# Optimization experiments

Measured on AMD Instinct MI355X. Metric: run time of the kernel, lower is better.

The kernel has to match this reference:

```python
import jax, jax.numpy as jnp
import numpy as np

D_MODEL = 512
NUM_HEADS = 8
D_K = D_MODEL // NUM_HEADS
SCALE = float(np.sqrt(D_K))


def setup_inputs() -> dict:
    key = jax.random.key(0)
    ks = jax.random.split(key, 11)
    B, S, D = 2, 4096, D_MODEL
    std = 1.0 / np.sqrt(D)
    return {
        "query": jax.random.normal(ks[0], (B, S, D), jnp.float32),
        "key": jax.random.normal(ks[1], (B, S, D), jnp.float32),
        "value": jax.random.normal(ks[2], (B, S, D), jnp.float32),
        "w_q": jax.random.normal(ks[3], (D, D), jnp.float32) * std,
        "b_q": jax.random.normal(ks[4], (D,), jnp.float32) * std,
        "w_k": jax.random.normal(ks[5], (D, D), jnp.float32) * std,
        "b_k": jax.random.normal(ks[6], (D,), jnp.float32) * std,
        "w_v": jax.random.normal(ks[7], (D, D), jnp.float32) * std,
        "b_v": jax.random.normal(ks[8], (D,), jnp.float32) * std,
        "w_o": jax.random.normal(ks[9], (D, D), jnp.float32) * std,
        "b_o": jax.random.normal(ks[10], (D,), jnp.float32) * std,
    }


def reference(query, key, value, w_q, b_q, w_k, b_k, w_v, b_v, w_o, b_o):
    B, S, D = query.shape
    H, Dk = NUM_HEADS, D_K
    # Linear projections (torch Linear: x @ W^T + b), split into heads -> [B,H,S,Dk]
    Q = (query @ w_q.T + b_q).reshape(B, S, H, Dk).transpose(0, 2, 1, 3)
    K = (key @ w_k.T + b_k).reshape(B, S, H, Dk).transpose(0, 2, 1, 3)
    V = (value @ w_v.T + b_v).reshape(B, S, H, Dk).transpose(0, 2, 1, 3)
    # [B,H,S,S] attention scores — intentionally materialized like the original
    scores = jnp.einsum("bhqd,bhkd->bhqk", Q, K) / SCALE
    attn = jax.nn.softmax(scores, axis=-1)  # dropout rate 0 in eval baseline
    attended = jnp.einsum("bhqk,bhkd->bhqd", attn, V)
    attended = attended.transpose(0, 2, 1, 3).reshape(B, S, D)
    return attended @ w_o.T + b_o
```

## Files before the change

### kernel.cpp

```cpp
#include <hip/hip_runtime.h>
#include <math.h>

#define D_MODEL 512
#define NHEADS 8
#define DK 64
#define BATCH 2
#define SEQ 4096
#define NIT 32
#define ATTN_SCALE 0.18033688011112043f
#define SPLIT_SCALE 2048.0f
#define INV_SPLIT  (1.0f/2048.0f)

typedef _Float16 half8 __attribute__((ext_vector_type(8)));
typedef __fp16 pkhalf2 __attribute__((ext_vector_type(2)));
typedef float f32x4 __attribute__((ext_vector_type(4)));

union Pk8 { _Float16 h[8]; uint4 u; };
union Pk4 { _Float16 h[4]; uint2 u; };
union Pkz { pkhalf2 h2[2]; uint2 u; };
union Un4 { uint2 u; _Float16 h[4]; };

#if __has_builtin(__builtin_amdgcn_exp2f)
#define EXP2F __builtin_amdgcn_exp2f
#else
#define EXP2F exp2f
#endif

#define MFMA16(a, b, c) __builtin_amdgcn_mfma_f32_16x16x32_f16((a), (b), (c), 0, 0, 0)

__device__ __forceinline__ void gload_lds16(const _Float16* g, _Float16* l) {
    __builtin_amdgcn_global_load_lds(
        (const __attribute__((address_space(1))) void*)g,
        (__attribute__((address_space(3))) void*)l, 16, 0, 0);
}

#define ABLK 4096
#define WBLK 256
__global__ __launch_bounds__(256)
void prep(const float* __restrict__ aq, const float* __restrict__ ak,
          const float* __restrict__ av,
          const float* __restrict__ wq, const float* __restrict__ wk,
          const float* __restrict__ wv, const float* __restrict__ wo,
          _Float16* __restrict__ dq, _Float16* __restrict__ dk,
          _Float16* __restrict__ dv,
          _Float16* __restrict__ hq, _Float16* __restrict__ hk,
          _Float16* __restrict__ hv, _Float16* __restrict__ ho) {
    int gid = blockIdx.x;
    const float* src;
    _Float16* hi;
    if (gid < 3 * ABLK) {
        const int w = gid / ABLK;
        gid -= w * ABLK;
        src = w == 0 ? aq : (w == 1 ? ak : av);
        hi  = w == 0 ? dq : (w == 1 ? dk : dv);
    } else {
        int g = gid - 3 * ABLK;
        const int w = g / WBLK;
        gid = g - w * WBLK;
        src = w == 0 ? wq : (w == 1 ? wk : (w == 2 ? wv : wo));
        hi  = w == 0 ? hq : (w == 1 ? hk : (w == 2 ? hv : ho));
    }
    const int i = (gid * 256 + threadIdx.x) * 4;
    float4 v = *(const float4*)(src + i);
    Pkz h;
    h.h2[0] = __builtin_amdgcn_cvt_pkrtz(v.x, v.y);
    h.h2[1] = __builtin_amdgcn_cvt_pkrtz(v.z, v.w);
    *(uint2*)(hi + i) = h.u;
}

__global__ __launch_bounds__(256)
void gemm_qkv(const _Float16* __restrict__ Aq, const _Float16* __restrict__ Ak,
              const _Float16* __restrict__ Av,
              const _Float16* __restrict__ Whq, const _Float16* __restrict__ Whk,
              const _Float16* __restrict__ Whv,
              const float* __restrict__ bq, const float* __restrict__ bk,
              const float* __restrict__ bv,
              _Float16* __restrict__ Qf, _Float16* __restrict__ Kf,
              _Float16* __restrict__ Vtf) {
    const int z = blockIdx.z;
    const _Float16* A    = z == 0 ? Aq  : (z == 1 ? Ak  : Av);
    const _Float16* Wh   = z == 0 ? Whq : (z == 1 ? Whk : Whv);
    const float*    bias = z == 0 ? bq  : (z == 1 ? bk  : bv);

    __shared__ __align__(16) _Float16 sA[2][128 * 64];
    __shared__ __align__(16) _Float16 sW[2][128 * 64];

    const int t    = threadIdx.x;
    const int lane = t & 63, wave = t >> 6;
    const int col  = lane & 15, quad = lane >> 4;
    const int wm   = (wave & 1) * 64, wn = (wave >> 1) * 64;
    const int m0   = blockIdx.y * 128, n0 = blockIdx.x * 128;

    const int subrow = lane >> 3;
    const int schunk = ((lane & 7) ^ subrow) * 8;

    #define STAGE_AW(K0, BUF)                                                        \
        do {                                                                          \
            _Pragma("unroll")                                                         \
            for (int j = 0; j < 4; ++j) {                                             \
                const int rw = wave * 32 + j * 8;                                     \
                gload_lds16(A  + (size_t)(m0 + rw + subrow) * 512 + (K0) + schunk,    \
                            &sA[BUF][rw * 64]);                                       \
                gload_lds16(Wh + (size_t)(n0 + rw + subrow) * 512 + (K0) + schunk,    \
                            &sW[BUF][rw * 64]);                                       \
            }                                                                         \
        } while (0)

    f32x4 acc[4][4] = {};

    STAGE_AW(0, 0);
    for (int ck = 0; ck < 8; ++ck) {
        const int cur = ck & 1;
        __syncthreads();
        if (ck + 1 < 8) STAGE_AW((ck + 1) * 64, cur ^ 1);

        #pragma unroll
        for (int kc = 0; kc < 2; ++kc) {
            const int pos = ((kc * 4 + quad) ^ (col & 7)) * 8;
            half8 af[4], wf[4];
            #pragma unroll
            for (int mt = 0; mt < 4; ++mt)
                af[mt] = *(const half8*)&sA[cur][(wm + mt * 16 + col) * 64 + pos];
            #pragma unroll
            for (int nt = 0; nt < 4; ++nt)
                wf[nt] = *(const half8*)&sW[cur][(wn + nt * 16 + col) * 64 + pos];
            #pragma unroll
            for (int mt = 0; mt < 4; ++mt)
                #pragma unroll
                for (int nt = 0; nt < 4; ++nt)
                    acc[mt][nt] = MFMA16(af[mt], wf[nt], acc[mt][nt]);
        }
    }

    float bv4[4];
    #pragma unroll
    for (int nt = 0; nt < 4; ++nt) bv4[nt] = bias[n0 + wn + nt * 16 + col];

    if (z < 2) {
        _Float16* Out = z == 0 ? Qf : Kf;
        const float alpha = z == 0 ? ATTN_SCALE : 1.0f;
        #pragma unroll
        for (int mt = 0; mt < 4; ++mt) {
            const int m = m0 + wm + mt * 16 + quad * 4;
            #pragma unroll
            for (int nt = 0; nt < 4; ++nt) {
                const int n = n0 + wn + nt * 16 + col;
                #pragma unroll
                for (int r = 0; r < 4; ++r)
                    Out[(size_t)(m + r) * 512 + n] = (_Float16)((acc[mt][nt][r] + bv4[nt]) * alpha);
            }
        }
    } else {
        #pragma unroll
        for (int mt = 0; mt < 4; ++mt) {
            const int m = m0 + wm + mt * 16 + quad * 4;
            const int b = m >> 12, s = m & (SEQ - 1);
            #pragma unroll
            for (int nt = 0; nt < 4; ++nt) {
                const int n = n0 + wn + nt * 16 + col;
                const int hh = n >> 6, d = n & (DK - 1);
                Pk4 p;
                #pragma unroll
                for (int r = 0; r < 4; ++r)
                    p.h[r] = (_Float16)(acc[mt][nt][r] + bv4[nt]);
                *(uint2*)&Vtf[((size_t)((b * NHEADS + hh) * DK + d)) * SEQ + s] = p.u;
            }
        }
    }
}

__global__ __launch_bounds__(256)
void attn_mfma(const _Float16* __restrict__ Qf, const _Float16* __restrict__ Kf,
               const _Float16* __restrict__ Vtf,
               _Float16* __restrict__ Op0, _Float16* __restrict__ Op1,
               float2* __restrict__ Ml) {
    __shared__ __align__(16) _Float16 sK[2][64 * 64];
    __shared__ __align__(16) _Float16 sV[64 * 64];
    __shared__ __align__(16) _Float16 sP[128 * 64];

    const int t    = threadIdx.x;
    const int lane = t & 63;
    const int wave = t >> 6;
    const int col  = lane & 15;
    const int quad = lane >> 4;

    const int strm = blockIdx.x;
    const int h  = strm & (NHEADS - 1);
    const int z  = strm >> 3;
    const int b  = z >> 1;
    const int sp = z & 1;
    const int q0 = blockIdx.y * 128;
    const int kBase = sp * (SEQ / 2);

    const size_t rowBase = (size_t)b * SEQ;
    const size_t vBase   = ((size_t)(b * NHEADS + h)) * DK * SEQ;

    const int subrow = lane >> 3;
    const int schunk = ((lane & 7) ^ subrow) * 8;
    const _Float16* kP[2];
    const _Float16* vP[2];
    #pragma unroll
    for (int j = 0; j < 2; ++j) {
        const int rw = wave * 16 + j * 8;
        kP[j] = Kf + (rowBase + kBase + rw + subrow) * 512 + h * 64 + schunk;
        vP[j] = Vtf + vBase + (size_t)(rw + subrow) * SEQ + kBase + schunk;
        gload_lds16(kP[j], &sK[0][rw * 64]);
        kP[j] += 64 * 512;
    }

    {
        uint4 qv[4];
        #pragma unroll
        for (int i2 = 0; i2 < 4; ++i2) {
            const int slot = t + i2 * 256;
            const int r = slot >> 3, sl = slot & 7;
            qv[i2] = *(const uint4*)(Qf + (rowBase + q0 + r) * 512 + h * 64 + sl * 8);
        }
        #pragma unroll
        for (int i2 = 0; i2 < 4; ++i2) {
            const int slot = t + i2 * 256;
            const int r = slot >> 3, sl = slot & 7;
            *(uint4*)&sP[r * 64 + (sl ^ (r & 7)) * 8] = qv[i2];
        }
    }
    __syncthreads();

    half8 qf[2][2];
    #pragma unroll
    for (int nt = 0; nt < 2; ++nt)
        #pragma unroll
        for (int kc = 0; kc < 2; ++kc)
            qf[nt][kc] = *(const half8*)&sP[(wave * 32 + nt * 16 + col) * 64 +
                                            ((kc * 4 + quad) ^ (col & 7)) * 8];

    _Float16* Ps = sP + wave * 32 * 64;
    const int pmsk = (col & 7) << 1;

    float m_r[2] = { -INFINITY, -INFINITY };
    float l_r[2] = { 0.0f, 0.0f };
    f32x4 of[4][2] = {};

    for (int itp = 0; itp < NIT; itp += 2) {
        #pragma unroll
        for (int cur = 0; cur < 2; ++cur) {
            const int it = itp + cur;
            __syncthreads();
            #pragma unroll
            for (int j = 0; j < 2; ++j) {
                const int rw = wave * 16 + j * 8;
                gload_lds16(vP[j], &sV[rw * 64]);
                vP[j] += 64;
            }
            if (it + 1 < NIT) {
                #pragma unroll
                for (int j = 0; j < 2; ++j) {
                    const int rw = wave * 16 + j * 8;
                    gload_lds16(kP[j], &sK[cur ^ 1][rw * 64]);
                    kP[j] += 64 * 512;
                }
            }

            f32x4 sf[4][2] = {};
            #pragma unroll
            for (int kc = 0; kc < 2; ++kc) {
                const int pos = ((kc * 4 + quad) ^ (col & 7)) * 8;
                #pragma unroll
                for (int kt = 0; kt < 4; ++kt) {
                    half8 kf = *(const half8*)&sK[cur][(kt * 16 + col) * 64 + pos];
                    #pragma unroll
                    for (int nt = 0; nt < 2; ++nt)
                        sf[kt][nt] = MFMA16(kf, qf[nt][kc], sf[kt][nt]);
                }
            }

            if (it == 0) {
                #pragma unroll
                for (int nt = 0; nt < 2; ++nt) {
                    float mx = sf[0][nt][0];
                    #pragma unroll
                    for (int kt = 0; kt < 4; ++kt)
                        #pragma unroll
                        for (int r = 0; r < 4; ++r)
                            mx = fmaxf(mx, sf[kt][nt][r]);
                    mx = fmaxf(mx, __shfl_xor(mx, 16));
                    mx = fmaxf(mx, __shfl_xor(mx, 32));
                    m_r[nt] = mx;
                }
            }

            float lrs[2];
            #pragma unroll
            for (int nt = 0; nt < 2; ++nt) {
                float ls = 0.0f;
                #pragma unroll
                for (int kt = 0; kt < 4; ++kt) {
                    const float p0 = EXP2F(sf[kt][nt][0] - m_r[nt]);
                    const float p1 = EXP2F(sf[kt][nt][1] - m_r[nt]);
                    const float p2 = EXP2F(sf[kt][nt][2] - m_r[nt]);
                    const float p3 = EXP2F(sf[kt][nt][3] - m_r[nt]);
                    ls += (p0 + p1) + (p2 + p3);
                    Pkz z2;
                    z2.h2[0] = __builtin_amdgcn_cvt_pkrtz(p0, p1);
                    z2.h2[1] = __builtin_amdgcn_cvt_pkrtz(p2, p3);
                    *(uint2*)&Ps[(nt * 16 + col) * 64 + ((kt * 4 + quad) ^ pmsk) * 4] = z2.u;
                }
                lrs[nt] = ls;
            }

            __syncthreads();

            #pragma unroll
            for (int kc = 0; kc < 2; ++kc) {
                half8 pf[2];
                #pragma unroll
                for (int nt = 0; nt < 2; ++nt)
                    pf[nt] = *(const half8*)&Ps[(nt * 16 + col) * 64 +
                                                ((kc * 8 + quad * 2) ^ pmsk) * 4];
                const int pos = ((kc * 4 + quad) ^ (col & 7)) * 8;
                #pragma unroll
                for (int dt = 0; dt < 4; ++dt) {
                    half8 vf = *(const half8*)&sV[(dt * 16 + col) * 64 + pos];
                    of[dt][0] = MFMA16(vf, pf[0], of[dt][0]);
                    of[dt][1] = MFMA16(vf, pf[1], of[dt][1]);
                }
            }

            l_r[0] += lrs[0];
            l_r[1] += lrs[1];

            if (__any(fmaxf(lrs[0], lrs[1]) > 1024.0f)) {
                #pragma unroll
                for (int nt = 0; nt < 2; ++nt) {
                    float mx = sf[0][nt][0];
                    #pragma unroll
                    for (int kt = 0; kt < 4; ++kt)
                        #pragma unroll
                        for (int r = 0; r < 4; ++r)
                            mx = fmaxf(mx, sf[kt][nt][r]);
                    mx = fmaxf(mx, __shfl_xor(mx, 16));
                    mx = fmaxf(mx, __shfl_xor(mx, 32));
                    if (mx > m_r[nt]) {
                        const float al = EXP2F(m_r[nt] - mx);
                        l_r[nt] *= al;
                        #pragma unroll
                        for (int dt = 0; dt < 4; ++dt)
                            #pragma unroll
                            for (int r = 0; r < 4; ++r)
                                of[dt][nt][r] *= al;
                        m_r[nt] = mx;
                    }
                }
            }
        }
    }

    _Float16* Opx = sp ? Op1 : Op0;
    #pragma unroll
    for (int nt = 0; nt < 2; ++nt) {
        float l = l_r[nt];
        l += __shfl_xor(l, 16);
        l += __shfl_xor(l, 32);
        const float inv = 1.0f / l;
        const int q = q0 + wave * 32 + nt * 16 + col;
        const size_t R = (size_t)b * SEQ + q;
        #pragma unroll
        for (int dt = 0; dt < 4; ++dt) {
            Pkz z2;
            z2.h2[0] = __builtin_amdgcn_cvt_pkrtz(of[dt][nt][0] * inv, of[dt][nt][1] * inv);
            z2.h2[1] = __builtin_amdgcn_cvt_pkrtz(of[dt][nt][2] * inv, of[dt][nt][3] * inv);
            *(uint2*)(Opx + R * 512 + h * 64 + dt * 16 + quad * 4) = z2.u;
        }
        if (quad == 0)
            Ml[(size_t)(sp * BATCH * SEQ) * NHEADS + R * NHEADS + h] = make_float2(m_r[nt], l);
    }
}

__global__ __launch_bounds__(256)
void attn_merge(const _Float16* __restrict__ Op0, const _Float16* __restrict__ Op1,
                const float2* __restrict__ Ml, _Float16* __restrict__ Oh) {
    const int i4 = (blockIdx.x * 256 + threadIdx.x) * 4;
    const int R = i4 >> 9;
    const int c = i4 & 511;
    const int h = c >> 6;

    const float2 ml1 = Ml[(size_t)R * NHEADS + h];
    const float2 ml2 = Ml[(size_t)(BATCH * SEQ) * NHEADS + (size_t)R * NHEADS + h];
    const float m = fmaxf(ml1.x, ml2.x);
    float w1 = EXP2F(ml1.x - m) * ml1.y;
    float w2 = EXP2F(ml2.x - m) * ml2.y;
    const float inv = 1.0f / (w1 + w2);
    w1 *= inv; w2 *= inv;

    Un4 a, bb;
    a.u  = *(const uint2*)(Op0 + (size_t)R * 512 + c);
    bb.u = *(const uint2*)(Op1 + (size_t)R * 512 + c);

    Pkz hh;
    hh.h2[0] = __builtin_amdgcn_cvt_pkrtz(w1 * (float)a.h[0] + w2 * (float)bb.h[0],
                                          w1 * (float)a.h[1] + w2 * (float)bb.h[1]);
    hh.h2[1] = __builtin_amdgcn_cvt_pkrtz(w1 * (float)a.h[2] + w2 * (float)bb.h[2],
                                          w1 * (float)a.h[3] + w2 * (float)bb.h[3]);
    *(uint2*)(Oh + (size_t)R * 512 + c) = hh.u;
}

__global__ __launch_bounds__(256)
void gemm_out(const _Float16* __restrict__ Ah, const _Float16* __restrict__ Wh,
              const float* __restrict__ bias, float* __restrict__ C) {
    __shared__ __align__(16) _Float16 sAh[2][128 * 64];
    __shared__ __align__(16) _Float16 sWh[2][64 * 64];

    const int t    = threadIdx.x;
    const int lane = t & 63, wave = t >> 6;
    const int col  = lane & 15, quad = lane >> 4;
    const int wm   = (wave & 1) * 64, wn = (wave >> 1) * 32;
    const int m0   = blockIdx.y * 128, n0 = blockIdx.x * 64;

    const int subrow = lane >> 3;
    const int schunk = ((lane & 7) ^ subrow) * 8;

    #define STAGE_OUT(K0, BUF)                                                       \
        do {                                                                          \
            _Pragma("unroll")                                                         \
            for (int j = 0; j < 4; ++j) {                                             \
                const int rw = wave * 32 + j * 8;                                     \
                gload_lds16(Ah + (size_t)(m0 + rw + subrow) * 512 + (K0) + schunk,    \
                            &sAh[BUF][rw * 64]);                                      \
            }                                                                         \
            _Pragma("unroll")                                                         \
            for (int j = 0; j < 2; ++j) {                                             \
                const int rw = wave * 16 + j * 8;                                     \
                gload_lds16(Wh + (size_t)(n0 + rw + subrow) * 512 + (K0) + schunk,    \
                            &sWh[BUF][rw * 64]);                                      \
            }                                                                         \
        } while (0)

    f32x4 acc[4][2] = {};

    STAGE_OUT(0, 0);
    for (int ck = 0; ck < 8; ++ck) {
        const int cur = ck & 1;
        __syncthreads();
        if (ck + 1 < 8) STAGE_OUT((ck + 1) * 64, cur ^ 1);

        #pragma unroll
        for (int kc = 0; kc < 2; ++kc) {
            const int pos = ((kc * 4 + quad) ^ (col & 7)) * 8;
            half8 ahf[4], whf[2];
            #pragma unroll
            for (int mt = 0; mt < 4; ++mt)
                ahf[mt] = *(const half8*)&sAh[cur][(wm + mt * 16 + col) * 64 + pos];
            #pragma unroll
            for (int nt = 0; nt < 2; ++nt)
                whf[nt] = *(const half8*)&sWh[cur][(wn + nt * 16 + col) * 64 + pos];
            #pragma unroll
            for (int mt = 0; mt < 4; ++mt)
                #pragma unroll
                for (int nt = 0; nt < 2; ++nt)
                    acc[mt][nt] = MFMA16(ahf[mt], whf[nt], acc[mt][nt]);
        }
    }

    float bv2[2];
    #pragma unroll
    for (int nt = 0; nt < 2; ++nt) bv2[nt] = bias[n0 + wn + nt * 16 + col];

    #pragma unroll
    for (int mt = 0; mt < 4; ++mt) {
        const int m = m0 + wm + mt * 16 + quad * 4;
        #pragma unroll
        for (int nt = 0; nt < 2; ++nt) {
            const int n = n0 + wn + nt * 16 + col;
            #pragma unroll
            for (int r = 0; r < 4; ++r)
                C[(size_t)(m + r) * 512 + n] = acc[mt][nt][r] + bv2[nt];
        }
    }
}

extern "C" void kernel_launch(void* const* d_in, const int* in_sizes, int n_in,
                              void* d_out, int out_size, void* d_ws, size_t ws_size,
                              hipStream_t stream) {
    const float* query = (const float*)d_in[0];
    const float* key   = (const float*)d_in[1];
    const float* value = (const float*)d_in[2];
    const float* w_q   = (const float*)d_in[3];
    const float* b_q   = (const float*)d_in[4];
    const float* w_k   = (const float*)d_in[5];
    const float* b_k   = (const float*)d_in[6];
    const float* w_v   = (const float*)d_in[7];
    const float* b_v   = (const float*)d_in[8];
    const float* w_o   = (const float*)d_in[9];
    const float* b_o   = (const float*)d_in[10];
    float* out = (float*)d_out;

    const int WN = D_MODEL * D_MODEL;
    const size_t plane = (size_t)BATCH * SEQ * D_MODEL;

    _Float16* base = (_Float16*)d_ws;
    _Float16* Aq16 = base;
    _Float16* Ak16 = Aq16 + plane;
    _Float16* Av16 = Ak16 + plane;
    _Float16* whq  = Av16 + plane;
    _Float16* whk  = whq + WN;
    _Float16* whv  = whk + WN;
    _Float16* who  = whv + WN;
    _Float16* Qf   = who + WN;
    _Float16* Kf   = Qf + plane;
    _Float16* Vtf  = Kf + plane;
    _Float16* Op1  = Vtf + plane;
    float2*   Ml   = (float2*)(Op1 + plane);
    _Float16* Oh   = Aq16;
    _Float16* Op0  = Av16;

    dim3 blk(256);

    hipLaunchKernelGGL(prep, dim3(3 * ABLK + 4 * WBLK), blk, 0, stream,
                       query, key, value, w_q, w_k, w_v, w_o,
                       Aq16, Ak16, Av16, whq, whk, whv, who);

    hipLaunchKernelGGL(gemm_qkv, dim3(D_MODEL / 128, BATCH * SEQ / 128, 3), blk, 0, stream,
                       Aq16, Ak16, Av16,
                       whq, whk, whv,
                       b_q, b_k, b_v, Qf, Kf, Vtf);

    hipLaunchKernelGGL(attn_mfma, dim3(NHEADS * BATCH * 2, SEQ / 128), blk, 0, stream,
                       Qf, Kf, Vtf, Op0, Op1, Ml);

    hipLaunchKernelGGL(attn_merge, dim3(BATCH * SEQ * D_MODEL / 4 / 256), blk, 0, stream,
                       Op0, Op1, Ml, Oh);

    hipLaunchKernelGGL(gemm_out, dim3(D_MODEL / 64, BATCH * SEQ / 128), blk, 0, stream,
                       Oh, who, b_o, out);
}
```

Baseline: 257.0 us.

## Double-buffer V tiles, per-wave P buffers, fold max into MFMA accumulator init

V tiles are now double-buffered and prefetched one iteration ahead together with K. The per-wave P staging drops to a 32x32 buffer written and read in two halves, which removes the block-wide barrier between softmax and PV. Q fragments load directly from global instead of through LDS, and the running max is subtracted by seeding the QK accumulator with -m. s_setprio hints wrap the MFMA sections. These aim to cut barriers and LDS traffic and to overlap loads, at the cost of more LDS for V and reliance on wave-local ordering of the P writes and reads.

```diff
diff --git a/kernel.cpp b/kernel.cpp
--- a/kernel.cpp
+++ b/kernel.cpp
@@ -8,8 +8,6 @@
 #define SEQ 4096
 #define NIT 32
 #define ATTN_SCALE 0.18033688011112043f
-#define SPLIT_SCALE 2048.0f
-#define INV_SPLIT  (1.0f/2048.0f)
 
 typedef _Float16 half8 __attribute__((ext_vector_type(8)));
 typedef __fp16 pkhalf2 __attribute__((ext_vector_type(2)));
@@ -32,6 +30,10 @@
     __builtin_amdgcn_global_load_lds(
         (const __attribute__((address_space(1))) void*)g,
         (__attribute__((address_space(3))) void*)l, 16, 0, 0);
+}
+
+__device__ __forceinline__ f32x4 splat4(float v) {
+    return (f32x4){v, v, v, v};
 }
 
 #define ABLK 4096
@@ -175,8 +177,8 @@
                _Float16* __restrict__ Op0, _Float16* __restrict__ Op1,
                float2* __restrict__ Ml) {
     __shared__ __align__(16) _Float16 sK[2][64 * 64];
-    __shared__ __align__(16) _Float16 sV[64 * 64];
-    __shared__ __align__(16) _Float16 sP[128 * 64];
+    __shared__ __align__(16) _Float16 sV[2][64 * 64];
+    __shared__ __align__(16) _Float16 sP[4][32 * 32];
 
     const int t    = threadIdx.x;
     const int lane = t & 63;
@@ -205,38 +207,25 @@
         kP[j] = Kf + (rowBase + kBase + rw + subrow) * 512 + h * 64 + schunk;
         vP[j] = Vtf + vBase + (size_t)(rw + subrow) * SEQ + kBase + schunk;
         gload_lds16(kP[j], &sK[0][rw * 64]);
+        gload_lds16(vP[j], &sV[0][rw * 64]);
         kP[j] += 64 * 512;
-    }
-
-    {
-        uint4 qv[4];
-        #pragma unroll
-        for (int i2 = 0; i2 < 4; ++i2) {
-            const int slot = t + i2 * 256;
-            const int r = slot >> 3, sl = slot & 7;
-            qv[i2] = *(const uint4*)(Qf + (rowBase + q0 + r) * 512 + h * 64 + sl * 8);
-        }
-        #pragma unroll
-        for (int i2 = 0; i2 < 4; ++i2) {
-            const int slot = t + i2 * 256;
-            const int r = slot >> 3, sl = slot & 7;
-            *(uint4*)&sP[r * 64 + (sl ^ (r & 7)) * 8] = qv[i2];
-        }
-    }
-    __syncthreads();
+        vP[j] += 64;
+    }
 
     half8 qf[2][2];
     #pragma unroll
     for (int nt = 0; nt < 2; ++nt)
         #pragma unroll
         for (int kc = 0; kc < 2; ++kc)
-            qf[nt][kc] = *(const half8*)&sP[(wave * 32 + nt * 16 + col) * 64 +
-                                            ((kc * 4 + quad) ^ (col & 7)) * 8];
-
-    _Float16* Ps = sP + wave * 32 * 64;
-    const int pmsk = (col & 7) << 1;
-
-    float m_r[2] = { -INFINITY, -INFINITY };
+            qf[nt][kc] = *(const half8*)(Qf +
+                (rowBase + q0 + wave * 32 + nt * 16 + col) * 512 +
+                h * 64 + (kc * 4 + quad) * 8);
+
+    _Float16* Ps = sP[wave];
+    const int c3   = (col & 3) << 1;
+    const int cmsk = col & 7;
+
+    float m_r[2] = { 0.0f, 0.0f };
     float l_r[2] = { 0.0f, 0.0f };
     f32x4 of[4][2] = {};
 
@@ -245,33 +234,35 @@
         for (int cur = 0; cur < 2; ++cur) {
             const int it = itp + cur;
             __syncthreads();
-            #pragma unroll
-            for (int j = 0; j < 2; ++j) {
-                const int rw = wave * 16 + j * 8;
-                gload_lds16(vP[j], &sV[rw * 64]);
-                vP[j] += 64;
-            }
             if (it + 1 < NIT) {
                 #pragma unroll
                 for (int j = 0; j < 2; ++j) {
                     const int rw = wave * 16 + j * 8;
                     gload_lds16(kP[j], &sK[cur ^ 1][rw * 64]);
+                    gload_lds16(vP[j], &sV[cur ^ 1][rw * 64]);
                     kP[j] += 64 * 512;
+                    vP[j] += 64;
                 }
             }
 
-            f32x4 sf[4][2] = {};
+            f32x4 sf[4][2];
+            #pragma unroll
+            for (int kt = 0; kt < 4; ++kt) {
+                sf[kt][0] = splat4(-m_r[0]);
+                sf[kt][1] = splat4(-m_r[1]);
+            }
+            __builtin_amdgcn_s_setprio(1);
             #pragma unroll
             for (int kc = 0; kc < 2; ++kc) {
-                const int pos = ((kc * 4 + quad) ^ (col & 7)) * 8;
+                const int pos = ((kc * 4 + quad) ^ cmsk) * 8;
                 #pragma unroll
                 for (int kt = 0; kt < 4; ++kt) {
                     half8 kf = *(const half8*)&sK[cur][(kt * 16 + col) * 64 + pos];
-                    #pragma unroll
-                    for (int nt = 0; nt < 2; ++nt)
-                        sf[kt][nt] = MFMA16(kf, qf[nt][kc], sf[kt][nt]);
+                    sf[kt][0] = MFMA16(kf, qf[0][kc], sf[kt][0]);
+                    sf[kt][1] = MFMA16(kf, qf[1][kc], sf[kt][1]);
                 }
             }
+            __builtin_amdgcn_s_setprio(0);
 
             if (it == 0) {
                 #pragma unroll
@@ -285,44 +276,48 @@
                     mx = fmaxf(mx, __shfl_xor(mx, 16));
                     mx = fmaxf(mx, __shfl_xor(mx, 32));
                     m_r[nt] = mx;
+                    #pragma unroll
+                    for (int kt = 0; kt < 4; ++kt)
+                        #pragma unroll
+                        for (int r = 0; r < 4; ++r)
+                            sf[kt][nt][r] -= mx;
                 }
             }
 
-            float lrs[2];
-            #pragma unroll
-            for (int nt = 0; nt < 2; ++nt) {
-                float ls = 0.0f;
-                #pragma unroll
-                for (int kt = 0; kt < 4; ++kt) {
-                    const float p0 = EXP2F(sf[kt][nt][0] - m_r[nt]);
-                    const float p1 = EXP2F(sf[kt][nt][1] - m_r[nt]);
-                    const float p2 = EXP2F(sf[kt][nt][2] - m_r[nt]);
-                    const float p3 = EXP2F(sf[kt][nt][3] - m_r[nt]);
-                    ls += (p0 + p1) + (p2 + p3);
-                    Pkz z2;
-                    z2.h2[0] = __builtin_amdgcn_cvt_pkrtz(p0, p1);
-                    z2.h2[1] = __builtin_amdgcn_cvt_pkrtz(p2, p3);
-                    *(uint2*)&Ps[(nt * 16 + col) * 64 + ((kt * 4 + quad) ^ pmsk) * 4] = z2.u;
+            float lrs[2] = { 0.0f, 0.0f };
+            #pragma unroll
+            for (int kh = 0; kh < 2; ++kh) {
+                #pragma unroll
+                for (int kt2 = 0; kt2 < 2; ++kt2) {
+                    const int kt = kh * 2 + kt2;
+                    #pragma unroll
+                    for (int nt = 0; nt < 2; ++nt) {
+                        const float p0 = EXP2F(sf[kt][nt][0]);
+                        const float p1 = EXP2F(sf[kt][nt][1]);
+                        const float p2 = EXP2F(sf[kt][nt][2]);
+                        const float p3 = EXP2F(sf[kt][nt][3]);
+                        lrs[nt] += (p0 + p1) + (p2 + p3);
+                        Pkz z2;
+                        z2.h2[0] = __builtin_amdgcn_cvt_pkrtz(p0, p1);
+                        z2.h2[1] = __builtin_amdgcn_cvt_pkrtz(p2, p3);
+                        *(uint2*)&Ps[(nt * 16 + col) * 32 +
+                                     (((kt2 * 4 + quad) ^ c3) << 2)] = z2.u;
+                    }
                 }
-                lrs[nt] = ls;
-            }
-
-            __syncthreads();
-
-            #pragma unroll
-            for (int kc = 0; kc < 2; ++kc) {
                 half8 pf[2];
                 #pragma unroll
                 for (int nt = 0; nt < 2; ++nt)
-                    pf[nt] = *(const half8*)&Ps[(nt * 16 + col) * 64 +
-                                                ((kc * 8 + quad * 2) ^ pmsk) * 4];
-                const int pos = ((kc * 4 + quad) ^ (col & 7)) * 8;
+                    pf[nt] = *(const half8*)&Ps[(nt * 16 + col) * 32 +
+                                                (((quad * 2) ^ c3) << 2)];
+                const int pos = ((kh * 4 + quad) ^ cmsk) * 8;
+                __builtin_amdgcn_s_setprio(1);
                 #pragma unroll
                 for (int dt = 0; dt < 4; ++dt) {
-                    half8 vf = *(const half8*)&sV[(dt * 16 + col) * 64 + pos];
+                    half8 vf = *(const half8*)&sV[cur][(dt * 16 + col) * 64 + pos];
                     of[dt][0] = MFMA16(vf, pf[0], of[dt][0]);
                     of[dt][1] = MFMA16(vf, pf[1], of[dt][1]);
                 }
+                __builtin_amdgcn_s_setprio(0);
             }
 
             l_r[0] += lrs[0];
@@ -339,15 +334,15 @@
                             mx = fmaxf(mx, sf[kt][nt][r]);
                     mx = fmaxf(mx, __shfl_xor(mx, 16));
                     mx = fmaxf(mx, __shfl_xor(mx, 32));
-                    if (mx > m_r[nt]) {
-                        const float al = EXP2F(m_r[nt] - mx);
+                    if (mx > 0.0f) {
+                        const float al = EXP2F(-mx);
                         l_r[nt] *= al;
                         #pragma unroll
                         for (int dt = 0; dt < 4; ++dt)
                             #pragma unroll
                             for (int r = 0; r < 4; ++r)
                                 of[dt][nt][r] *= al;
-                        m_r[nt] = mx;
+                        m_r[nt] += mx;
                     }
                 }
             }
```

Result: no change. 261.2 us (+1.6%).
